# Optimization experiments

Hardware: AMD Instinct MI355X
Metric: run time of the kernel (lower is better)

The kernel has to match this reference:

```python
import jax, jax.numpy as jnp
import numpy as np

NUM_HEADS = 32
NUM_KV_HEADS = 8
HEAD_DIM = 128
NEG_INF = -1e9


def rotate_half(x):
    x1, x2 = jnp.split(x, 2, axis=-1)
    return jnp.concatenate([-x2, x1], axis=-1)


def setup_inputs() -> dict:
    key = jax.random.key(0)
    ks = jax.random.split(key, 8)
    B, S, H = 2, 2048, 4096
    hidden_states = jax.random.normal(ks[0], (B, S, H), jnp.float32) * 0.02
    # additive causal mask [1,1,S,S]: 0 on/below diagonal, -1e9 above
    causal = jnp.tril(jnp.ones((S, S), bool))
    attention_mask = jnp.where(causal, 0.0, NEG_INF)[None, None, :, :].astype(jnp.float32)
    # RoPE tables (theta=500000 style), shape [1,S,head_dim]
    inv_freq = 1.0 / (500000.0 ** (np.arange(0, HEAD_DIM, 2, dtype=np.float32) / HEAD_DIM))
    t = np.arange(S, dtype=np.float32)
    freqs = np.outer(t, inv_freq)  # [S, head_dim/2]
    emb = np.concatenate([freqs, freqs], axis=-1)  # [S, head_dim]
    cos = jnp.asarray(np.cos(emb))[None]
    sin = jnp.asarray(np.sin(emb))[None]
    scale = 0.02
    wq = jax.random.normal(ks[1], (NUM_HEADS * HEAD_DIM, H), jnp.float32) * scale
    wk = jax.random.normal(ks[2], (NUM_KV_HEADS * HEAD_DIM, H), jnp.float32) * scale
    wv = jax.random.normal(ks[3], (NUM_KV_HEADS * HEAD_DIM, H), jnp.float32) * scale
    wo = jax.random.normal(ks[4], (H, NUM_HEADS * HEAD_DIM), jnp.float32) * scale
    return {"hidden_states": hidden_states, "attention_mask": attention_mask,
            "cos": cos, "sin": sin, "wq": wq, "wk": wk, "wv": wv, "wo": wo}


def reference(hidden_states, attention_mask, cos, sin, wq, wk, wv, wo):
    B, S, H = hidden_states.shape
    nh, nkv, hd = NUM_HEADS, NUM_KV_HEADS, HEAD_DIM
    groups = nh // nkv
    # QKV projections (bias=False)
    q = jnp.einsum('bsh,dh->bsd', hidden_states, wq).reshape(B, S, nh, hd).transpose(0, 2, 1, 3)
    k = jnp.einsum('bsh,dh->bsd', hidden_states, wk).reshape(B, S, nkv, hd).transpose(0, 2, 1, 3)
    v = jnp.einsum('bsh,dh->bsd', hidden_states, wv).reshape(B, S, nkv, hd).transpose(0, 2, 1, 3)
    # RoPE: cos/sin [1,S,hd] -> broadcast over head dim [1,1,S,hd]
    c = cos[:, None, :, :]
    s = sin[:, None, :, :]
    q = q * c + rotate_half(q) * s
    k = k * c + rotate_half(k) * s
    # GQA: repeat_kv
    k = jnp.repeat(k, groups, axis=1)  # [B,nh,S,hd]
    v = jnp.repeat(v, groups, axis=1)
    # SDPA with additive mask
    scores = jnp.einsum('bhqd,bhkd->bhqk', q, k) / jnp.sqrt(jnp.float32(hd))
    scores = scores + attention_mask[:, :, :, :k.shape[2]]
    attn = jax.nn.softmax(scores, axis=-1)
    out = jnp.einsum('bhqk,bhkd->bhqd', attn, v)  # [B,nh,S,hd]
    out = out.transpose(0, 2, 1, 3).reshape(B, S, nh * hd)
    return jnp.einsum('bsd,hd->bsh', out, wo)
```

## Files before the change

kernel.cpp:

```cpp
#include <hip/hip_runtime.h>
#include <hip/hip_bf16.h>

typedef __attribute__((ext_vector_type(8))) __bf16 bf16x8;
typedef __attribute__((ext_vector_type(4))) float f32x4;
typedef __attribute__((ext_vector_type(16))) float f32x16;
typedef __attribute__((ext_vector_type(4))) unsigned int u32x4;

#define SEQ 2048
#define NH 32
#define NKV 8
#define HD 128

__device__ __forceinline__ ushort f2bf(float f) {
  unsigned u = __builtin_bit_cast(unsigned, f);
  unsigned r = (u + 0x7fffu + ((u >> 16) & 1u)) >> 16;
  return (ushort)r;
}
__device__ __forceinline__ float bf2f(ushort h) {
  return __builtin_bit_cast(float, ((unsigned)h) << 16);
}
__device__ __forceinline__ unsigned cvt_pk_bf16(float lo, float hi) {
  unsigned r;
  asm("v_cvt_pk_bf16_f32 %0, %1, %2" : "=v"(r) : "v"(lo), "v"(hi));
  return r;
}
__device__ __forceinline__ float exp2_fast(float x) {
  float r;
  asm("v_exp_f32 %0, %1" : "=v"(r) : "v"(x));
  return r;
}
__device__ __forceinline__ void gload16(const void* g, void* l) {
  __builtin_amdgcn_global_load_lds(
      (const __attribute__((address_space(1))) void*)g,
      (__attribute__((address_space(3))) void*)l, 16, 0, 0);
}

__global__ __launch_bounds__(256) void f2bf5_kernel(const float4* __restrict__ hs,
                                                    const float4* __restrict__ wq,
                                                    const float4* __restrict__ wk,
                                                    const float4* __restrict__ wv,
                                                    const float4* __restrict__ wo,
                                                    ushort4* __restrict__ out) {
  unsigned i = blockIdx.x * 256 + threadIdx.x;
  const float4* src;
  unsigned j;
  if (i < 4194304u) { src = hs; j = i; }
  else if (i < 8388608u) { src = wq; j = i - 4194304u; }
  else if (i < 9437184u) { src = wk; j = i - 8388608u; }
  else if (i < 10485760u) { src = wv; j = i - 9437184u; }
  else { src = wo; j = i - 10485760u; }
  float4 v = src[j];
  ushort4 o;
  o.x = f2bf(v.x); o.y = f2bf(v.y); o.z = f2bf(v.z); o.w = f2bf(v.w);
  out[i] = o;
}

template <int OUTF32>
__global__ __launch_bounds__(256) void gemm_bt_kernel(const ushort* __restrict__ A,
                                                      const ushort* __restrict__ B,
                                                      void* __restrict__ C,
                                                      int M, int N, int K) {
  __shared__ ushort As[2][128 * 32];
  __shared__ ushort Bs[2][128 * 32];
  const int tid = threadIdx.x;
  const int w = tid >> 6, l = tid & 63;
  const int lr = l & 15, lc = l >> 4;
  const int bx = blockIdx.x, by = blockIdx.y;
  const int wr = w >> 1, wc = w & 1;

  f32x4 z = {0.f, 0.f, 0.f, 0.f};
  f32x4 acc[4][4];
#pragma unroll
  for (int i = 0; i < 4; ++i)
#pragma unroll
    for (int j = 0; j < 4; ++j) acc[i][j] = z;

  const ushort* aSrc = A + (size_t)(by * 128 + 32 * w + (l >> 2)) * K + (l & 3) * 8;
  const ushort* bSrc = B + (size_t)(bx * 128 + 32 * w + (l >> 2)) * K + (l & 3) * 8;
  const int ldsOff = (32 * w) * 32;

#pragma unroll
  for (int q = 0; q < 2; ++q) {
    gload16(aSrc + (size_t)q * 16 * K, &As[0][ldsOff + q * 512]);
    gload16(bSrc + (size_t)q * 16 * K, &Bs[0][ldsOff + q * 512]);
  }
  __syncthreads();

  const int nk = K >> 5;
  int cur = 0;
  for (int kt = 0; kt < nk; ++kt) {
    if (kt + 1 < nk) {
      const ushort* a2 = aSrc + (size_t)(kt + 1) * 32;
      const ushort* b2 = bSrc + (size_t)(kt + 1) * 32;
#pragma unroll
      for (int q = 0; q < 2; ++q) {
        gload16(a2 + (size_t)q * 16 * K, &As[cur ^ 1][ldsOff + q * 512]);
        gload16(b2 + (size_t)q * 16 * K, &Bs[cur ^ 1][ldsOff + q * 512]);
      }
    }
    bf16x8 af[4], bfr[4];
#pragma unroll
    for (int i = 0; i < 4; ++i)
      af[i] = *(const bf16x8*)&As[cur][(64 * wr + 16 * i + lr) * 32 + lc * 8];
#pragma unroll
    for (int j = 0; j < 4; ++j)
      bfr[j] = *(const bf16x8*)&Bs[cur][(64 * wc + 16 * j + lr) * 32 + lc * 8];
#pragma unroll
    for (int i = 0; i < 4; ++i)
#pragma unroll
      for (int j = 0; j < 4; ++j)
        acc[i][j] = __builtin_amdgcn_mfma_f32_16x16x32_bf16(af[i], bfr[j], acc[i][j], 0, 0, 0);
    __syncthreads();
    cur ^= 1;
  }

#pragma unroll
  for (int i = 0; i < 4; ++i)
#pragma unroll
    for (int j = 0; j < 4; ++j) {
      int row = by * 128 + 64 * wr + 16 * i + lc * 4;
      int col = bx * 128 + 64 * wc + 16 * j + lr;
#pragma unroll
      for (int r = 0; r < 4; ++r) {
        if (OUTF32)
          ((float*)C)[(size_t)(row + r) * N + col] = acc[i][j][r];
        else
          ((ushort*)C)[(size_t)(row + r) * N + col] = f2bf(acc[i][j][r]);
      }
    }
}

template <int OUTF32>
__global__ __launch_bounds__(512, 2) void gemm256_kernel(const ushort* __restrict__ A,
                                                         const ushort* __restrict__ B,
                                                         void* __restrict__ C,
                                                         int M, int N, int K) {
  __shared__ ushort As[2][256 * 64];
  __shared__ ushort Bs[2][256 * 64];
  const int tid = threadIdx.x;
  const int w = tid >> 6, l = tid & 63;
  const int lr = l & 15, lc = l >> 4;
  const int wr = w >> 2, wc = w & 3;

  const int nbx = N >> 8;
  const int cpx = gridDim.x >> 3;
  const int sw = (blockIdx.x & 7) * cpx + (blockIdx.x >> 3);
  const int bx = sw % nbx, by = sw / nbx;

  const ushort* Asrc = A + (size_t)(by * 256) * K;
  const ushort* Bsrc = B + (size_t)(bx * 256) * K;

  f32x4 z = {0.f, 0.f, 0.f, 0.f};
  f32x4 acc[8][4];
#pragma unroll
  for (int m = 0; m < 8; ++m)
#pragma unroll
    for (int n = 0; n < 4; ++n) acc[m][n] = z;

  const int NK = K >> 6;

  auto stage = [&](int kt2, int s) {
    if (kt2 >= NK) return;
    const int mat = s >> 1, half = s & 1;
    const ushort* g = mat ? Bsrc : Asrc;
    char* lb = (char*)(mat ? &Bs[kt2 & 1][0] : &As[kt2 & 1][0]) + half * 16384 + w * 1024;
#pragma unroll
    for (int i = 0; i < 2; ++i) {
      int row = half * 128 + i * 64 + w * 8 + (l >> 3);
      int csw = ((l & 7) * 16) ^ ((row & 7) << 4);
      gload16(g + (size_t)row * K + kt2 * 64 + (csw >> 1), lb + i * 8192);
    }
  };

  stage(0, 0); stage(0, 1); stage(0, 2); stage(0, 3);
  stage(1, 0);

  bf16x8 af[4][2], bfr[4][2];
  for (int kt = 0; kt < NK; ++kt) {
    const char* Ab = (const char*)&As[kt & 1][0];
    const char* Bb = (const char*)&Bs[kt & 1][0];
    if (kt + 1 < NK) asm volatile("s_waitcnt vmcnt(2)" ::: "memory");
    else             asm volatile("s_waitcnt vmcnt(0)" ::: "memory");
    asm volatile("s_barrier" ::: "memory");

#pragma unroll
    for (int m = 0; m < 4; ++m) {
      int row = wr * 128 + m * 16 + lr;
#pragma unroll
      for (int ks = 0; ks < 2; ++ks)
        af[m][ks] = *(const bf16x8*)(Ab + row * 128 + ((ks * 64 + lc * 16) ^ ((row & 7) << 4)));
    }
#pragma unroll
    for (int n = 0; n < 2; ++n) {
      int row = wc * 64 + n * 16 + lr;
#pragma unroll
      for (int ks = 0; ks < 2; ++ks)
        bfr[n][ks] = *(const bf16x8*)(Bb + row * 128 + ((ks * 64 + lc * 16) ^ ((row & 7) << 4)));
    }
    stage(kt + 1, 1);
    __builtin_amdgcn_s_setprio(1);
#pragma unroll
    for (int m = 0; m < 4; ++m)
#pragma unroll
      for (int n = 0; n < 2; ++n)
#pragma unroll
        for (int ks = 0; ks < 2; ++ks)
          acc[m][n] = __builtin_amdgcn_mfma_f32_16x16x32_bf16(af[m][ks], bfr[n][ks], acc[m][n], 0, 0, 0);
    __builtin_amdgcn_s_setprio(0);
    asm volatile("s_barrier" ::: "memory");

#pragma unroll
    for (int n = 2; n < 4; ++n) {
      int row = wc * 64 + n * 16 + lr;
#pragma unroll
      for (int ks = 0; ks < 2; ++ks)
        bfr[n][ks] = *(const bf16x8*)(Bb + row * 128 + ((ks * 64 + lc * 16) ^ ((row & 7) << 4)));
    }
    stage(kt + 1, 2);
    __builtin_amdgcn_s_setprio(1);
#pragma unroll
    for (int m = 0; m < 4; ++m)
#pragma unroll
      for (int n = 2; n < 4; ++n)
#pragma unroll
        for (int ks = 0; ks < 2; ++ks)
          acc[m][n] = __builtin_amdgcn_mfma_f32_16x16x32_bf16(af[m][ks], bfr[n][ks], acc[m][n], 0, 0, 0);
    __builtin_amdgcn_s_setprio(0);
    asm volatile("s_barrier" ::: "memory");

#pragma unroll
    for (int m = 0; m < 4; ++m) {
      int row = wr * 128 + (m + 4) * 16 + lr;
#pragma unroll
      for (int ks = 0; ks < 2; ++ks)
        af[m][ks] = *(const bf16x8*)(Ab + row * 128 + ((ks * 64 + lc * 16) ^ ((row & 7) << 4)));
    }
    stage(kt + 1, 3);
    __builtin_amdgcn_s_setprio(1);
#pragma unroll
    for (int m = 0; m < 4; ++m)
#pragma unroll
      for (int n = 0; n < 2; ++n)
#pragma unroll
        for (int ks = 0; ks < 2; ++ks)
          acc[m + 4][n] = __builtin_amdgcn_mfma_f32_16x16x32_bf16(af[m][ks], bfr[n][ks], acc[m + 4][n], 0, 0, 0);
    __builtin_amdgcn_s_setprio(0);
    asm volatile("s_barrier" ::: "memory");

    stage(kt + 2, 0);
    __builtin_amdgcn_s_setprio(1);
#pragma unroll
    for (int m = 0; m < 4; ++m)
#pragma unroll
      for (int n = 2; n < 4; ++n)
#pragma unroll
        for (int ks = 0; ks < 2; ++ks)
          acc[m + 4][n] = __builtin_amdgcn_mfma_f32_16x16x32_bf16(af[m][ks], bfr[n][ks], acc[m + 4][n], 0, 0, 0);
    __builtin_amdgcn_s_setprio(0);
  }

#pragma unroll
  for (int m = 0; m < 8; ++m)
#pragma unroll
    for (int n = 0; n < 4; ++n) {
      int row = by * 256 + wr * 128 + m * 16 + lc * 4;
      int col = bx * 256 + wc * 64 + n * 16 + lr;
#pragma unroll
      for (int r = 0; r < 4; ++r) {
        if (OUTF32)
          ((float*)C)[(size_t)(row + r) * N + col] = acc[m][n][r];
        else
          ((ushort*)C)[(size_t)(row + r) * N + col] = f2bf(acc[m][n][r]);
      }
    }
}

__global__ __launch_bounds__(256) void rope_kernel(const ushort* __restrict__ in, int ld,
                                                   const float* __restrict__ cosb,
                                                   const float* __restrict__ sinb,
                                                   ushort* __restrict__ out,
                                                   int hshift, float scale) {
  int idx = blockIdx.x * 256 + threadIdx.x;
  int d = idx & 63;
  int nh = 1 << hshift;
  int h = (idx >> 6) & (nh - 1);
  int rowg = idx >> (6 + hshift);
  int s = rowg & (SEQ - 1);
  int b = rowg >> 11;
  const ushort* p = in + (size_t)rowg * ld + h * HD + d;
  float x = bf2f(p[0]), y = bf2f(p[64]);
  float c = cosb[s * HD + d], sn = sinb[s * HD + d];
  ushort* qo = out + (((size_t)(b * nh + h)) * SEQ + s) * HD + d;
  qo[0] = f2bf((x * c - y * sn) * scale);
  qo[64] = f2bf((y * c + x * sn) * scale);
}

__global__ __launch_bounds__(256) void vtrans_kernel(const ushort* __restrict__ vin,
                                                     ushort* __restrict__ vout) {
  __shared__ ushort t[64][66];
  const int s0 = blockIdx.x * 64;
  const int c0 = blockIdx.y * 64;
  const int b = blockIdx.z;
  const int tx = threadIdx.x & 63;
  const int ty = threadIdx.x >> 6;
#pragma unroll
  for (int rr = 0; rr < 64; rr += 4) {
    int r = rr + ty;
    t[r][tx] = vin[((size_t)(b * SEQ + s0 + r)) * 2048 + 1024 + c0 + tx];
  }
  __syncthreads();
#pragma unroll
  for (int rr = 0; rr < 64; rr += 4) {
    int c = rr + ty;
    int cg = c0 + c;
    int kvh = cg >> 7, d = cg & 127;
    vout[(((size_t)(b * NKV + kvh)) * HD + d) * SEQ + s0 + tx] = t[tx][c];
  }
}

__global__ __launch_bounds__(512, 2) void attn_kernel(const ushort* __restrict__ Qh,
                                                      const ushort* __restrict__ Kh,
                                                      const ushort* __restrict__ Vt,
                                                      ushort* __restrict__ Out) {
  __shared__ ushort Kl[2][64 * 128];
  __shared__ ushort Vl[128 * 64];

  const int tid = threadIdx.x;
  const int w = tid >> 6, l = tid & 63;
  const int lq = l & 31;
  const int hl = l >> 5;
  const int g = w >> 2;
  const int wl = w & 3;

  const int n = blockIdx.x;
  const int xcd = n & 7, i = n >> 3;
  const int qpi = i & 7;
  const int h2 = (i >> 3) & 3;
  const int pp = 2 * xcd + (i >> 5);
  const int bb = pp >> 3, kvh = pp & 7;
  const int hh = kvh * 4 + h2;
  const int bh = bb * 32 + hh;
  const int qt = g ? (15 - qpi) : qpi;
  const int q0 = qt * 128;
  const int wrow0 = q0 + 32 * wl;
  const int qrow = wrow0 + lq;

  const ushort* Kbase = Kh + ((size_t)(bb * NKV + kvh) * SEQ) * HD;
  const ushort* Vbase = Vt + ((size_t)(bb * NKV + kvh) * HD) * SEQ;

  bf16x8 qf[8];
  {
    const ushort* qrp = Qh + ((size_t)bh * SEQ + qrow) * HD + 8 * hl;
#pragma unroll
    for (int s8 = 0; s8 < 8; ++s8) qf[s8] = *(const bf16x8*)(qrp + 16 * s8);
  }

  f32x16 o[4];
#pragma unroll
  for (int db = 0; db < 4; ++db)
#pragma unroll
    for (int i2 = 0; i2 < 16; ++i2) o[db][i2] = 0.f;
  float m_run = -1e30f, l_run = 0.f;

  const int ntw = 2 * qt + (wl >> 1) + 1;
  const int ntb = 2 * (15 - qpi) + 2;

  auto stageK = [&](int buf, int t) {
    const int kv0 = t * 64;
#pragma unroll
    for (int q = 0; q < 2; ++q) {
      int c = 2 * w + q;
      int row = c * 4 + (l >> 4);
      int cs = ((l & 15) ^ (row & 7)) * 8;
      gload16(Kbase + ((size_t)(kv0 + row)) * HD + cs, &Kl[buf][c * 512]);
    }
  };
  auto stageV = [&](int t) {
    const int kv0 = t * 64;
#pragma unroll
    for (int q = 0; q < 2; ++q) {
      int c = 2 * w + q;
      int row = c * 8 + (l >> 3);
      int cs = ((l & 7) ^ (row & 7)) * 8;
      gload16(Vbase + (size_t)row * SEQ + kv0 + cs, &Vl[c * 512]);
    }
  };

  stageK(0, 0);
  __syncthreads();

  int cur = 0;
  for (int t = 0; t < ntb; ++t) {
    const int kv0 = t * 64;
    stageV(t);
    if (t + 1 < ntb) stageK(cur ^ 1, t + 1);

    f32x16 sacc[2];
    unsigned pw[2][8];
    const int swz = lq & 7;
    const bool act = (t < ntw);
    if (act) {
#pragma unroll
      for (int b2 = 0; b2 < 2; ++b2)
#pragma unroll
        for (int i2 = 0; i2 < 16; ++i2) sacc[b2][i2] = 0.f;

      __builtin_amdgcn_s_setprio(1);
#pragma unroll
      for (int s8 = 0; s8 < 8; ++s8) {
#pragma unroll
        for (int b2 = 0; b2 < 2; ++b2) {
          int row = 32 * b2 + lq;
          bf16x8 kf = *(const bf16x8*)((const char*)&Kl[cur][0] + row * 256 +
                                       (((2 * s8 + hl) ^ swz) << 4));
          sacc[b2] = __builtin_amdgcn_mfma_f32_32x32x16_bf16(kf, qf[s8], sacc[b2], 0, 0, 0);
        }
      }
      __builtin_amdgcn_s_setprio(0);

      if (t == ntw - 1) {
#pragma unroll
        for (int b2 = 0; b2 < 2; ++b2)
#pragma unroll
          for (int r2 = 0; r2 < 16; ++r2) {
            int kv = kv0 + 32 * b2 + (r2 & 3) + 8 * (r2 >> 2) + 4 * hl;
            if (kv > qrow) sacc[b2][r2] = -1e30f;
          }
      }

      float tm[8];
#pragma unroll
      for (int r2 = 0; r2 < 8; ++r2)
        tm[r2] = fmaxf(fmaxf(sacc[0][r2], sacc[0][r2 + 8]),
                       fmaxf(sacc[1][r2], sacc[1][r2 + 8]));
#pragma unroll
      for (int s2 = 4; s2; s2 >>= 1)
#pragma unroll
        for (int r2 = 0; r2 < s2; ++r2) tm[r2] = fmaxf(tm[r2], tm[r2 + s2]);
      float mx = fmaxf(tm[0], __shfl_xor(tm[0], 32));

      if (__any(mx > m_run + 8.0f)) {
        float mn = fmaxf(m_run, mx);
        float sc = exp2_fast(m_run - mn);
        m_run = mn;
        l_run *= sc;
#pragma unroll
        for (int db = 0; db < 4; ++db) o[db] *= sc;
      }

#pragma unroll
      for (int b2 = 0; b2 < 2; ++b2)
#pragma unroll
        for (int r2 = 0; r2 < 16; ++r2) sacc[b2][r2] = exp2_fast(sacc[b2][r2] - m_run);
      float ts[8];
#pragma unroll
      for (int r2 = 0; r2 < 8; ++r2)
        ts[r2] = (sacc[0][r2] + sacc[0][r2 + 8]) + (sacc[1][r2] + sacc[1][r2 + 8]);
#pragma unroll
      for (int s2 = 4; s2; s2 >>= 1)
#pragma unroll
        for (int r2 = 0; r2 < s2; ++r2) ts[r2] += ts[r2 + s2];
      l_run += ts[0] + __shfl_xor(ts[0], 32);

#pragma unroll
      for (int b2 = 0; b2 < 2; ++b2)
#pragma unroll
        for (int i2 = 0; i2 < 8; ++i2)
          pw[b2][i2] = cvt_pk_bf16(sacc[b2][2 * i2], sacc[b2][2 * i2 + 1]);
    }

    if (t + 1 < ntb) asm volatile("s_waitcnt vmcnt(2)" ::: "memory");
    else             asm volatile("s_waitcnt vmcnt(0)" ::: "memory");
    __builtin_amdgcn_s_barrier();
    __builtin_amdgcn_sched_barrier(0);

    if (act) {
#pragma unroll
      for (int s = 0; s < 4; ++s) {
        const int b2 = s >> 1, bs = 4 * (s & 1);
        unsigned wA = pw[b2][bs], wB = pw[b2][bs + 1], wC = pw[b2][bs + 2], wD = pw[b2][bs + 3];
        unsigned s1 = hl ? wA : wC, s2v = hl ? wB : wD;
        unsigned rx1 = (unsigned)__shfl_xor((int)s1, 32);
        unsigned rx2 = (unsigned)__shfl_xor((int)s2v, 32);
        u32x4 fw = {hl ? rx1 : wA, hl ? rx2 : wB, hl ? wC : rx1, hl ? wD : rx2};
        bf16x8 pfrag = __builtin_bit_cast(bf16x8, fw);
        bf16x8 vf[4];
#pragma unroll
        for (int db = 0; db < 4; ++db) {
          int row = 32 * db + lq;
          vf[db] = *(const bf16x8*)((const char*)&Vl[0] + row * 128 +
                                    (((2 * s + hl) ^ swz) << 4));
        }
        __builtin_amdgcn_s_setprio(1);
#pragma unroll
        for (int db = 0; db < 4; ++db)
          o[db] = __builtin_amdgcn_mfma_f32_32x32x16_bf16(vf[db], pfrag, o[db], 0, 0, 0);
        __builtin_amdgcn_s_setprio(0);
      }
    }
    __syncthreads();
    cur ^= 1;
  }

  const float inv = 1.0f / l_run;
  ushort* outp = Out + ((size_t)bb * SEQ + qrow) * (NH * HD) + hh * HD;
#pragma unroll
  for (int db = 0; db < 4; ++db)
#pragma unroll
    for (int i2 = 0; i2 < 8; ++i2) {
      unsigned wrd = cvt_pk_bf16(o[db][2 * i2] * inv, o[db][2 * i2 + 1] * inv);
      int d = 32 * db + 2 * (i2 & 1) + 8 * (i2 >> 1) + 4 * hl;
      *(unsigned*)(outp + d) = wrd;
    }
}

extern "C" void kernel_launch(void* const* d_in, const int* in_sizes, int n_in,
                              void* d_out, int out_size, void* d_ws, size_t ws_size,
                              hipStream_t stream) {
  const float* hs = (const float*)d_in[0];
  const float* cosb = (const float*)d_in[2];
  const float* sinb = (const float*)d_in[3];
  const float* wq = (const float*)d_in[4];
  const float* wk = (const float*)d_in[5];
  const float* wv = (const float*)d_in[6];
  const float* wo = (const float*)d_in[7];

  char* ws = (char*)d_ws;
  ushort* hs_bf = (ushort*)(ws);
  ushort* wq_bf = (ushort*)(ws + 33554432);
  ushort* wk_bf = (ushort*)(ws + 67108864);
  ushort* wo_bf = (ushort*)(ws + 83886080);
  ushort* q_lin = (ushort*)(ws + 117440512);
  ushort* kv_lin = (ushort*)(ws + 150994944);
  ushort* Qh = hs_bf;
  ushort* Kh = wq_bf;
  ushort* Vt = (ushort*)(ws + 41943040);
  ushort* attn_out = q_lin;

  f2bf5_kernel<<<57344, 256, 0, stream>>>((const float4*)hs, (const float4*)wq,
                                          (const float4*)wk, (const float4*)wv,
                                          (const float4*)wo, (ushort4*)ws);

  gemm256_kernel<0><<<256, 512, 0, stream>>>(hs_bf, wq_bf, q_lin, 4096, 4096, 4096);
  gemm_bt_kernel<0><<<dim3(16, 32), 256, 0, stream>>>(hs_bf, wk_bf, kv_lin, 4096, 2048, 4096);

  rope_kernel<<<32768, 256, 0, stream>>>(q_lin, 4096, cosb, sinb, Qh, 5,
                                         0.08838834764831845f * 1.4426950408889634f);
  rope_kernel<<<8192, 256, 0, stream>>>(kv_lin, 2048, cosb, sinb, Kh, 3, 1.0f);
  vtrans_kernel<<<dim3(32, 16, 2), 256, 0, stream>>>(kv_lin, Vt);

  attn_kernel<<<512, 512, 0, stream>>>(Qh, Kh, Vt, attn_out);

  gemm256_kernel<1><<<256, 512, 0, stream>>>(attn_out, wo_bf, d_out, 4096, 4096, 4096);
}
```

Baseline: 533.1 us.

## Double-buffer V in attention and merge RoPE and V-transpose into one launch

The attention loop now prefetches both K and V for the next KV tile into double-buffered LDS. This removes the mid-iteration vmcnt wait and barrier that previously stalled on the current tile's V load before the PV matmuls. Separately, the Q RoPE, K RoPE and V transpose kernels become one launch, with block-index ranges selecting the role, to cut launch overhead. The extra V buffer raises LDS per block to 64KB, which may limit occupancy. The remaining wait for the prefetch relies on the end-of-loop __syncthreads.

```diff
diff --git a/kernel.cpp b/kernel.cpp
--- a/kernel.cpp
+++ b/kernel.cpp
@@ -275,46 +275,56 @@
     }
 }
 
-__global__ __launch_bounds__(256) void rope_kernel(const ushort* __restrict__ in, int ld,
-                                                   const float* __restrict__ cosb,
-                                                   const float* __restrict__ sinb,
-                                                   ushort* __restrict__ out,
-                                                   int hshift, float scale) {
-  int idx = blockIdx.x * 256 + threadIdx.x;
-  int d = idx & 63;
-  int nh = 1 << hshift;
-  int h = (idx >> 6) & (nh - 1);
-  int rowg = idx >> (6 + hshift);
-  int s = rowg & (SEQ - 1);
-  int b = rowg >> 11;
-  const ushort* p = in + (size_t)rowg * ld + h * HD + d;
-  float x = bf2f(p[0]), y = bf2f(p[64]);
-  float c = cosb[s * HD + d], sn = sinb[s * HD + d];
-  ushort* qo = out + (((size_t)(b * nh + h)) * SEQ + s) * HD + d;
-  qo[0] = f2bf((x * c - y * sn) * scale);
-  qo[64] = f2bf((y * c + x * sn) * scale);
-}
-
-__global__ __launch_bounds__(256) void vtrans_kernel(const ushort* __restrict__ vin,
-                                                     ushort* __restrict__ vout) {
+__global__ __launch_bounds__(256) void relayout_kernel(const ushort* __restrict__ q_lin,
+                                                       const ushort* __restrict__ kv_lin,
+                                                       const float* __restrict__ cosb,
+                                                       const float* __restrict__ sinb,
+                                                       ushort* __restrict__ Qh,
+                                                       ushort* __restrict__ Kh,
+                                                       ushort* __restrict__ Vt,
+                                                       float qscale) {
   __shared__ ushort t[64][66];
-  const int s0 = blockIdx.x * 64;
-  const int c0 = blockIdx.y * 64;
-  const int b = blockIdx.z;
-  const int tx = threadIdx.x & 63;
-  const int ty = threadIdx.x >> 6;
-#pragma unroll
-  for (int rr = 0; rr < 64; rr += 4) {
-    int r = rr + ty;
-    t[r][tx] = vin[((size_t)(b * SEQ + s0 + r)) * 2048 + 1024 + c0 + tx];
-  }
-  __syncthreads();
-#pragma unroll
-  for (int rr = 0; rr < 64; rr += 4) {
-    int c = rr + ty;
-    int cg = c0 + c;
-    int kvh = cg >> 7, d = cg & 127;
-    vout[(((size_t)(b * NKV + kvh)) * HD + d) * SEQ + s0 + tx] = t[tx][c];
+  const unsigned bid = blockIdx.x;
+  if (bid < 40960u) {
+    const bool isQ = bid < 32768u;
+    const ushort* in = isQ ? q_lin : kv_lin;
+    ushort* out = isQ ? Qh : Kh;
+    const int ld = isQ ? 4096 : 2048;
+    const int hshift = isQ ? 5 : 3;
+    const float scale = isQ ? qscale : 1.0f;
+    int idx = (isQ ? bid : (bid - 32768u)) * 256 + threadIdx.x;
+    int d = idx & 63;
+    int nh = 1 << hshift;
+    int h = (idx >> 6) & (nh - 1);
+    int rowg = idx >> (6 + hshift);
+    int s = rowg & (SEQ - 1);
+    int b = rowg >> 11;
+    const ushort* p = in + (size_t)rowg * ld + h * HD + d;
+    float x = bf2f(p[0]), y = bf2f(p[64]);
+    float c = cosb[s * HD + d], sn = sinb[s * HD + d];
+    ushort* qo = out + (((size_t)(b * nh + h)) * SEQ + s) * HD + d;
+    qo[0] = f2bf((x * c - y * sn) * scale);
+    qo[64] = f2bf((y * c + x * sn) * scale);
+  } else {
+    unsigned i = bid - 40960u;
+    const int s0 = (i & 31) * 64;
+    const int c0 = ((i >> 5) & 15) * 64;
+    const int b = i >> 9;
+    const int tx = threadIdx.x & 63;
+    const int ty = threadIdx.x >> 6;
+#pragma unroll
+    for (int rr = 0; rr < 64; rr += 4) {
+      int r = rr + ty;
+      t[r][tx] = kv_lin[((size_t)(b * SEQ + s0 + r)) * 2048 + 1024 + c0 + tx];
+    }
+    __syncthreads();
+#pragma unroll
+    for (int rr = 0; rr < 64; rr += 4) {
+      int c = rr + ty;
+      int cg = c0 + c;
+      int kvh = cg >> 7, d = cg & 127;
+      Vt[(((size_t)(b * NKV + kvh)) * HD + d) * SEQ + s0 + tx] = t[tx][c];
+    }
   }
 }
 
@@ -323,7 +333,7 @@
                                                       const ushort* __restrict__ Vt,
                                                       ushort* __restrict__ Out) {
   __shared__ ushort Kl[2][64 * 128];
-  __shared__ ushort Vl[128 * 64];
+  __shared__ ushort Vl[2][128 * 64];
 
   const int tid = threadIdx.x;
   const int w = tid >> 6, l = tid & 63;
@@ -365,7 +375,7 @@
   const int ntw = 2 * qt + (wl >> 1) + 1;
   const int ntb = 2 * (15 - qpi) + 2;
 
-  auto stageK = [&](int buf, int t) {
+  auto stageKV = [&](int buf, int t) {
     const int kv0 = t * 64;
 #pragma unroll
     for (int q = 0; q < 2; ++q) {
@@ -374,37 +384,31 @@
       int cs = ((l & 15) ^ (row & 7)) * 8;
       gload16(Kbase + ((size_t)(kv0 + row)) * HD + cs, &Kl[buf][c * 512]);
     }
-  };
-  auto stageV = [&](int t) {
-    const int kv0 = t * 64;
 #pragma unroll
     for (int q = 0; q < 2; ++q) {
       int c = 2 * w + q;
       int row = c * 8 + (l >> 3);
       int cs = ((l & 7) ^ (row & 7)) * 8;
-      gload16(Vbase + (size_t)row * SEQ + kv0 + cs, &Vl[c * 512]);
+      gload16(Vbase + (size_t)row * SEQ + kv0 + cs, &Vl[buf][c * 512]);
     }
   };
 
-  stageK(0, 0);
+  stageKV(0, 0);
   __syncthreads();
 
   int cur = 0;
   for (int t = 0; t < ntb; ++t) {
     const int kv0 = t * 64;
-    stageV(t);
-    if (t + 1 < ntb) stageK(cur ^ 1, t + 1);
-
-    f32x16 sacc[2];
-    unsigned pw[2][8];
-    const int swz = lq & 7;
-    const bool act = (t < ntw);
-    if (act) {
+    if (t + 1 < ntb) stageKV(cur ^ 1, t + 1);
+
+    if (t < ntw) {
+      f32x16 sacc[2];
 #pragma unroll
       for (int b2 = 0; b2 < 2; ++b2)
 #pragma unroll
         for (int i2 = 0; i2 < 16; ++i2) sacc[b2][i2] = 0.f;
 
+      const int swz = lq & 7;
       __builtin_amdgcn_s_setprio(1);
 #pragma unroll
       for (int s8 = 0; s8 < 8; ++s8) {
@@ -462,19 +466,13 @@
         for (int r2 = 0; r2 < s2; ++r2) ts[r2] += ts[r2 + s2];
       l_run += ts[0] + __shfl_xor(ts[0], 32);
 
+      unsigned pw[2][8];
 #pragma unroll
       for (int b2 = 0; b2 < 2; ++b2)
 #pragma unroll
         for (int i2 = 0; i2 < 8; ++i2)
           pw[b2][i2] = cvt_pk_bf16(sacc[b2][2 * i2], sacc[b2][2 * i2 + 1]);
-    }
-
-    if (t + 1 < ntb) asm volatile("s_waitcnt vmcnt(2)" ::: "memory");
-    else             asm volatile("s_waitcnt vmcnt(0)" ::: "memory");
-    __builtin_amdgcn_s_barrier();
-    __builtin_amdgcn_sched_barrier(0);
-
-    if (act) {
+
 #pragma unroll
       for (int s = 0; s < 4; ++s) {
         const int b2 = s >> 1, bs = 4 * (s & 1);
@@ -488,7 +486,7 @@
 #pragma unroll
         for (int db = 0; db < 4; ++db) {
           int row = 32 * db + lq;
-          vf[db] = *(const bf16x8*)((const char*)&Vl[0] + row * 128 +
+          vf[db] = *(const bf16x8*)((const char*)&Vl[cur][0] + row * 128 +
                                     (((2 * s + hl) ^ swz) << 4));
         }
         __builtin_amdgcn_s_setprio(1);
@@ -544,10 +542,8 @@
   gemm256_kernel<0><<<256, 512, 0, stream>>>(hs_bf, wq_bf, q_lin, 4096, 4096, 4096);
   gemm_bt_kernel<0><<<dim3(16, 32), 256, 0, stream>>>(hs_bf, wk_bf, kv_lin, 4096, 2048, 4096);
 
-  rope_kernel<<<32768, 256, 0, stream>>>(q_lin, 4096, cosb, sinb, Qh, 5,
-                                         0.08838834764831845f * 1.4426950408889634f);
-  rope_kernel<<<8192, 256, 0, stream>>>(kv_lin, 2048, cosb, sinb, Kh, 3, 1.0f);
-  vtrans_kernel<<<dim3(32, 16, 2), 256, 0, stream>>>(kv_lin, Vt);
+  relayout_kernel<<<41984, 256, 0, stream>>>(q_lin, kv_lin, cosb, sinb, Qh, Kh, Vt,
+                                             0.08838834764831845f * 1.4426950408889634f);
 
   attn_kernel<<<512, 512, 0, stream>>>(Qh, Kh, Vt, attn_out);
 
```

Result: no change. 525.0 us, median of 3 (-1.5%).
